# Kernel optimization log

Hardware: AMD Instinct MI355X
Metric: run time of the kernel (lower is better)

Reference implementation:

```python
import jax, jax.numpy as jnp
import numpy as np


def setup_inputs() -> dict:
    B, C, N = 8, 512, 2048
    ks = jax.random.split(jax.random.key(0), 5)
    return {
        "src_embedding": jax.random.normal(ks[0], (B, C, N), jnp.float32),
        "tgt_embedding": jax.random.normal(ks[1], (B, C, N), jnp.float32),
        "src": jax.random.normal(ks[2], (B, 3, N), jnp.float32),
        "tgt": jax.random.normal(ks[3], (B, 3, N), jnp.float32),
        "temperature": jnp.ones((B, 1), jnp.float32),
        "gumbel_u": jax.random.uniform(ks[4], (B * N, N), jnp.float32),
    }


def reference(src_embedding, tgt_embedding, src, tgt, temperature, gumbel_u):
    B, C, N = src_embedding.shape
    # cross-attention scores: [B, N, N]
    scores = jnp.einsum('bcn,bcm->bnm', src_embedding, tgt_embedding) / jnp.sqrt(jnp.float32(C))
    scores = scores.reshape(B * N, N)
    tau = jnp.repeat(temperature.reshape(B, 1, 1), N, axis=1).reshape(-1, 1)  # [B*N, 1]
    # gumbel-softmax (hard=True, straight-through)
    u = jnp.clip(gumbel_u, 1e-6, 1.0 - 1e-6)
    g = -jnp.log(-jnp.log(u))
    y_soft = jax.nn.softmax((scores + g) / tau, axis=-1)
    idx = jnp.argmax(y_soft, axis=-1)
    y_hard = jax.nn.one_hot(idx, N, dtype=y_soft.dtype)
    scores_st = y_hard - jax.lax.stop_gradient(y_soft) + y_soft
    scores_st = scores_st.reshape(B, N, N)
    # soft correspondences: tgt @ scores^T -> [B, 3, N]
    src_corr = jnp.einsum('bcm,bnm->bcn', tgt, scores_st)
    src_mean = src.mean(axis=2, keepdims=True)
    corr_mean = src_corr.mean(axis=2, keepdims=True)
    src_c = src - src_mean
    corr_c = src_corr - corr_mean
    # 3x3 covariance per batch
    H = jnp.einsum('bcn,bdn->bcd', src_c, corr_c)
    uS, s, vh = jnp.linalg.svd(H)
    v = jnp.swapaxes(vh, -1, -2)
    uT = jnp.swapaxes(uS, -1, -2)
    r = v @ uT
    det = jax.lax.stop_gradient(jnp.linalg.det(r))  # torch code uses .item(): constant
    d = jnp.stack([jnp.ones_like(det), jnp.ones_like(det), det], axis=-1)  # [B, 3]
    R = (v * d[:, None, :]) @ uT  # v @ diag([1,1,det]) @ u^T
    t = jnp.einsum('bij,bjk->bik', -R, src_mean) + corr_mean
    return R, t.reshape(B, 3)
```

## Files before the change

### kernel.cpp

```cpp
#include <hip/hip_runtime.h>
#include <hip/hip_fp16.h>
#include <math.h>

#define NB 8
#define NC 512
#define NN 2048

typedef __attribute__((ext_vector_type(8))) _Float16 f16x8;
typedef __attribute__((ext_vector_type(4))) float f32x4;

union U8 { uint32_t u[4]; f16x8 v; };

__device__ __forceinline__ unsigned f2mono(float v) {
    unsigned b = __float_as_uint(v);
    return (b & 0x80000000u) ? ~b : (b | 0x80000000u);
}

__device__ __forceinline__ uint32_t packsplit(float a) {
    __half h = __float2half(a);
    float hf = __half2float(h);
    __half lo = __float2half(a - hf);
    return (uint32_t)__half_as_ushort(h) | ((uint32_t)__half_as_ushort(lo) << 16);
}

__device__ __forceinline__ void g2lds16(const void* g, void* l) {
    __builtin_amdgcn_global_load_lds(
        (const __attribute__((address_space(1))) void*)g,
        (__attribute__((address_space(3))) void*)l, 16, 0, 0);
}

extern "C" __global__ __launch_bounds__(256)
void prepack(const float* __restrict__ srcE, const float* __restrict__ tgtE,
             unsigned short* __restrict__ hiA, unsigned short* __restrict__ loA,
             unsigned short* __restrict__ hiB, unsigned short* __restrict__ loB)
{
    const float* in = blockIdx.y ? tgtE : srcE;
    unsigned short* hi = blockIdx.y ? hiB : hiA;
    unsigned short* lo = blockIdx.y ? loB : loA;
    const int t  = blockIdx.x;
    const int b  = t >> 7;
    const int kt = (t >> 3) & 15;
    const int nt = t & 7;
    const int k0 = kt * 32, n0 = nt * 256;

    const int n_l = threadIdx.x;
    const int n   = n0 + n_l;
    const int s2  = (n >> 1) & 3;
    const float* gin = in + (size_t)b * (NC * NN) + (size_t)k0 * NN + n;

    float v[32];
#pragma unroll
    for (int k = 0; k < 32; ++k) v[k] = gin[(size_t)k * NN];

    uint32_t hw[16], lw[16];
#pragma unroll
    for (int j = 0; j < 16; ++j) {
        __half h0 = __float2half(v[2*j]);
        __half h1 = __float2half(v[2*j+1]);
        float  d0 = v[2*j]   - __half2float(h0);
        float  d1 = v[2*j+1] - __half2float(h1);
        hw[j] = (uint32_t)__half_as_ushort(h0) | ((uint32_t)__half_as_ushort(h1) << 16);
        lw[j] = (uint32_t)__half_as_ushort(__float2half(d0)) |
                ((uint32_t)__half_as_ushort(__float2half(d1)) << 16);
    }
    const size_t rowbase = ((size_t)b * NN + n) * NC;
#pragma unroll
    for (int o = 0; o < 4; ++o) {
        const int P = kt * 4 + (o ^ s2);
        uint4 qh, ql;
        qh.x = hw[4*o+0]; qh.y = hw[4*o+1]; qh.z = hw[4*o+2]; qh.w = hw[4*o+3];
        ql.x = lw[4*o+0]; ql.y = lw[4*o+1]; ql.z = lw[4*o+2]; ql.w = lw[4*o+3];
        *(uint4*)(hi + rowbase + (size_t)P * 8) = qh;
        *(uint4*)(lo + rowbase + (size_t)P * 8) = ql;
    }
}

extern "C" __global__ __launch_bounds__(256, 2)
void scores_argmax_sb(const unsigned short* __restrict__ hiA, const unsigned short* __restrict__ loA,
                      const unsigned short* __restrict__ hiB, const unsigned short* __restrict__ loB,
                      const float* __restrict__ gum,
                      unsigned long long* __restrict__ best)
{
    __shared__ unsigned short lds[4][4096];

    const int id = blockIdx.x;
    const int flat = (id & 7) * 256 + (id >> 3);
    const int mt = flat & 15;
    const int nt = (flat >> 4) & 15;
    const int b  = flat >> 8;
    const int n0 = nt * 128, m0 = mt * 128;

    const int tid = threadIdx.x;
    const int wv = tid >> 6;
    const int l  = tid & 63;
    const int wn = wv >> 1, wm = wv & 1;
    const int row16 = l & 15, h = l >> 4;
    const int s2 = (row16 >> 1) & 3;
    const int fo = (h ^ s2) * 8;

    const unsigned short* gp;
    int pan;
    if (wv == 0)      { gp = hiA; pan = n0; }
    else if (wv == 1) { gp = loA; pan = n0; }
    else if (wv == 2) { gp = hiB; pan = m0; }
    else              { gp = loB; pan = m0; }
    gp += ((size_t)b * NN + pan) * NC;
    const unsigned short* gl = gp + (size_t)(l >> 2) * NC + (l & 3) * 8;

    f32x4 acc[4][4];
#pragma unroll
    for (int i = 0; i < 4; ++i)
#pragma unroll
        for (int j = 0; j < 4; ++j)
            acc[i][j] = (f32x4){0.f, 0.f, 0.f, 0.f};

#pragma unroll 1
    for (int t = 0; t < 16; ++t) {
        __syncthreads();
        {
            const unsigned short* s_ = gl + (size_t)t * 32;
#pragma unroll
            for (int c = 0; c < 8; ++c)
                g2lds16(s_ + (size_t)c * 16 * NC, &lds[wv][c * 512]);
        }
        __syncthreads();

        f16x8 bh[4], bl[4];
#pragma unroll
        for (int ms = 0; ms < 4; ++ms) {
            const int r_ = wm * 64 + ms * 16 + row16;
            bh[ms] = *(const f16x8*)&lds[2][r_ * 32 + fo];
            bl[ms] = *(const f16x8*)&lds[3][r_ * 32 + fo];
        }
#pragma unroll
        for (int ns = 0; ns < 4; ++ns) {
            const int r_ = wn * 64 + ns * 16 + row16;
            const f16x8 ah = *(const f16x8*)&lds[0][r_ * 32 + fo];
            const f16x8 al = *(const f16x8*)&lds[1][r_ * 32 + fo];
#pragma unroll
            for (int ms = 0; ms < 4; ++ms) {
                acc[ns][ms] = __builtin_amdgcn_mfma_f32_16x16x32_f16(ah, bh[ms], acc[ns][ms], 0, 0, 0);
                acc[ns][ms] = __builtin_amdgcn_mfma_f32_16x16x32_f16(al, bh[ms], acc[ns][ms], 0, 0, 0);
                acc[ns][ms] = __builtin_amdgcn_mfma_f32_16x16x32_f16(ah, bl[ms], acc[ns][ms], 0, 0, 0);
            }
        }
    }

    const float SCL = 0.044194173824159216f;
#pragma unroll
    for (int ns = 0; ns < 4; ++ns) {
#pragma unroll
        for (int reg = 0; reg < 4; ++reg) {
            const int n = n0 + wn * 64 + ns * 16 + h * 4 + reg;
            const float* gr = gum + ((size_t)(b * NN + n)) * NN + m0 + wm * 64 + row16;
            unsigned long long bp = 0ULL;
#pragma unroll
            for (int ms = 0; ms < 4; ++ms) {
                float u = gr[ms * 16];
                u = fminf(fmaxf(u, 1e-6f), 1.0f - 1e-6f);
                const float g = -__logf(-__logf(u));
                const float val = fmaf(acc[ns][ms][reg], SCL, g);
                const int m = m0 + wm * 64 + ms * 16 + row16;
                const unsigned long long p =
                    ((unsigned long long)f2mono(val) << 32) | (unsigned)(NN - 1 - m);
                if (p > bp) bp = p;
            }
#pragma unroll
            for (int off = 8; off > 0; off >>= 1) {
                const unsigned long long o = __shfl_xor(bp, off, 16);
                if (o > bp) bp = o;
            }
            if (row16 == 0) atomicMax(&best[(size_t)b * NN + n], bp);
        }
    }
}

extern "C" __global__ __launch_bounds__(256, 2)
void scores_argmax(const float* __restrict__ srcE,
                   const float* __restrict__ tgtE,
                   const float* __restrict__ gum,
                   const float* __restrict__ temp,
                   unsigned long long* __restrict__ best)
{
    __shared__ uint32_t As[128 * 32];
    __shared__ uint32_t Bs[128 * 32];
    const int id = blockIdx.x;
    const int flat = (id & 7) * 256 + (id >> 3);
    const int mt = flat & 15;
    const int nt = (flat >> 4) & 15;
    const int b  = flat >> 8;
    const int n0 = nt * 128, m0 = mt * 128;

    const int tid = threadIdx.x;
    const int wv = tid >> 6;
    const int l  = tid & 63;
    const int wn = wv >> 1, wm = wv & 1;
    const int row16 = l & 15, h = l >> 4;

    const int snb = 4 * (tid & 31);
    const int skb = tid >> 5;
    const uint32_t sswz = (uint32_t)(tid & 7) << 2;

    const float* Ag = srcE + (size_t)b * NC * NN + n0 + snb;
    const float* Bg = tgtE + (size_t)b * NC * NN + m0 + snb;

    float4 pA[4], pB[4];
#pragma unroll
    for (int r = 0; r < 4; ++r) {
        pA[r] = *(const float4*)(Ag + (size_t)(skb + 8 * r) * NN);
        pB[r] = *(const float4*)(Bg + (size_t)(skb + 8 * r) * NN);
    }

    f32x4 acc[4][4];
#pragma unroll
    for (int i = 0; i < 4; ++i)
#pragma unroll
        for (int j = 0; j < 4; ++j)
            acc[i][j] = (f32x4){0.f, 0.f, 0.f, 0.f};

    for (int k0 = 0; k0 < NC; k0 += 32) {
        __syncthreads();
#pragma unroll
        for (int r = 0; r < 4; ++r) {
            const int k = skb + 8 * r;
            const uint32_t kx = (uint32_t)k ^ sswz;
            uint32_t* ap = &As[snb * 32 + kx];
            uint32_t* bq = &Bs[snb * 32 + kx];
            ap[0]  = packsplit(pA[r].x); ap[32] = packsplit(pA[r].y);
            ap[64] = packsplit(pA[r].z); ap[96] = packsplit(pA[r].w);
            bq[0]  = packsplit(pB[r].x); bq[32] = packsplit(pB[r].y);
            bq[64] = packsplit(pB[r].z); bq[96] = packsplit(pB[r].w);
        }
        if (k0 + 32 < NC) {
#pragma unroll
            for (int r = 0; r < 4; ++r) {
                pA[r] = *(const float4*)(Ag + (size_t)(k0 + 32 + skb + 8 * r) * NN);
                pB[r] = *(const float4*)(Bg + (size_t)(k0 + 32 + skb + 8 * r) * NN);
            }
        }
        __syncthreads();

        U8 bfh[4], bfl[4];
#pragma unroll
        for (int ms = 0; ms < 4; ++ms) {
            const int m_loc = wm * 64 + ms * 16 + row16;
            const uint32_t swz = (uint32_t)((ms * 4 + (row16 >> 2)) & 7) << 2;
            const int base = m_loc * 32;
            const uint4 r0 = *(const uint4*)&Bs[base + (((uint32_t)(h * 8 + 0)) ^ swz)];
            const uint4 r1 = *(const uint4*)&Bs[base + (((uint32_t)(h * 8 + 4)) ^ swz)];
            bfh[ms].u[0] = __builtin_amdgcn_perm(r0.y, r0.x, 0x05040100u);
            bfh[ms].u[1] = __builtin_amdgcn_perm(r0.w, r0.z, 0x05040100u);
            bfh[ms].u[2] = __builtin_amdgcn_perm(r1.y, r1.x, 0x05040100u);
            bfh[ms].u[3] = __builtin_amdgcn_perm(r1.w, r1.z, 0x05040100u);
            bfl[ms].u[0] = __builtin_amdgcn_perm(r0.y, r0.x, 0x07060302u);
            bfl[ms].u[1] = __builtin_amdgcn_perm(r0.w, r0.z, 0x07060302u);
            bfl[ms].u[2] = __builtin_amdgcn_perm(r1.y, r1.x, 0x07060302u);
            bfl[ms].u[3] = __builtin_amdgcn_perm(r1.w, r1.z, 0x07060302u);
        }

#pragma unroll
        for (int ns = 0; ns < 4; ++ns) {
            const int n_loc = wn * 64 + ns * 16 + row16;
            const uint32_t swz = (uint32_t)((ns * 4 + (row16 >> 2)) & 7) << 2;
            const int base = n_loc * 32;
            const uint4 r0 = *(const uint4*)&As[base + (((uint32_t)(h * 8 + 0)) ^ swz)];
            const uint4 r1 = *(const uint4*)&As[base + (((uint32_t)(h * 8 + 4)) ^ swz)];
            U8 ah, al;
            ah.u[0] = __builtin_amdgcn_perm(r0.y, r0.x, 0x05040100u);
            ah.u[1] = __builtin_amdgcn_perm(r0.w, r0.z, 0x05040100u);
            ah.u[2] = __builtin_amdgcn_perm(r1.y, r1.x, 0x05040100u);
            ah.u[3] = __builtin_amdgcn_perm(r1.w, r1.z, 0x05040100u);
            al.u[0] = __builtin_amdgcn_perm(r0.y, r0.x, 0x07060302u);
            al.u[1] = __builtin_amdgcn_perm(r0.w, r0.z, 0x07060302u);
            al.u[2] = __builtin_amdgcn_perm(r1.y, r1.x, 0x07060302u);
            al.u[3] = __builtin_amdgcn_perm(r1.w, r1.z, 0x07060302u);
#pragma unroll
            for (int ms = 0; ms < 4; ++ms) {
                acc[ns][ms] = __builtin_amdgcn_mfma_f32_16x16x32_f16(ah.v, bfh[ms].v, acc[ns][ms], 0, 0, 0);
                acc[ns][ms] = __builtin_amdgcn_mfma_f32_16x16x32_f16(al.v, bfh[ms].v, acc[ns][ms], 0, 0, 0);
                acc[ns][ms] = __builtin_amdgcn_mfma_f32_16x16x32_f16(ah.v, bfl[ms].v, acc[ns][ms], 0, 0, 0);
            }
        }
    }

    const float SCL = 0.044194173824159216f;
    const float tau = temp[b];
#pragma unroll
    for (int ns = 0; ns < 4; ++ns) {
#pragma unroll
        for (int reg = 0; reg < 4; ++reg) {
            const int n = n0 + wn * 64 + ns * 16 + h * 4 + reg;
            const float* gr = gum + ((size_t)(b * NN + n)) * NN + m0 + wm * 64 + row16;
            unsigned long long bp = 0ULL;
#pragma unroll
            for (int ms = 0; ms < 4; ++ms) {
                float u = gr[ms * 16];
                u = fminf(fmaxf(u, 1e-6f), 1.0f - 1e-6f);
                const float g = -logf(-logf(u));
                const float val = (acc[ns][ms][reg] * SCL + g) / tau;
                const int m = m0 + wm * 64 + ms * 16 + row16;
                const unsigned long long p =
                    ((unsigned long long)f2mono(val) << 32) | (unsigned)(NN - 1 - m);
                if (p > bp) bp = p;
            }
#pragma unroll
            for (int off = 8; off > 0; off >>= 1) {
                const unsigned long long o = __shfl_xor(bp, off, 16);
                if (o > bp) bp = o;
            }
            if (row16 == 0) atomicMax(&best[(size_t)b * NN + n], bp);
        }
    }
}

__device__ __forceinline__ double det3(const double M[3][3]) {
    return M[0][0] * (M[1][1] * M[2][2] - M[1][2] * M[2][1])
         - M[0][1] * (M[1][0] * M[2][2] - M[1][2] * M[2][0])
         + M[0][2] * (M[1][0] * M[2][1] - M[1][1] * M[2][0]);
}

extern "C" __global__ __launch_bounds__(1024)
void assemble(const float* __restrict__ src, const float* __restrict__ tgt,
              const unsigned long long* __restrict__ best, float* __restrict__ out)
{
    const int b = blockIdx.x;
    const int tid = threadIdx.x;
    float P[9] = {}, Ss[3] = {}, Sc[3] = {};
    for (int n = tid; n < NN; n += 1024) {
        const int m = (NN - 1) - (int)(unsigned)(best[(size_t)b * NN + n] & 0xffffffffu);
        float sv[3], cv[3];
#pragma unroll
        for (int c = 0; c < 3; ++c) {
            sv[c] = src[((size_t)b * 3 + c) * NN + n];
            cv[c] = tgt[((size_t)b * 3 + c) * NN + m];
            Ss[c] += sv[c];
            Sc[c] += cv[c];
        }
#pragma unroll
        for (int c = 0; c < 3; ++c)
#pragma unroll
            for (int d = 0; d < 3; ++d)
                P[c * 3 + d] = fmaf(sv[c], cv[d], P[c * 3 + d]);
    }

    float vals[15];
#pragma unroll
    for (int i = 0; i < 9; ++i) vals[i] = P[i];
#pragma unroll
    for (int i = 0; i < 3; ++i) { vals[9 + i] = Ss[i]; vals[12 + i] = Sc[i]; }

    __shared__ float red[16][15];
    const int lane = tid & 63, wv = tid >> 6;
#pragma unroll
    for (int i = 0; i < 15; ++i) {
        float v = vals[i];
        for (int off = 32; off > 0; off >>= 1) v += __shfl_down(v, off, 64);
        if (lane == 0) red[wv][i] = v;
    }
    __syncthreads();

    if (tid == 0) {
        double tot[15];
        for (int i = 0; i < 15; ++i) {
            double s = 0.0;
            for (int wq = 0; wq < 16; ++wq) s += (double)red[wq][i];
            tot[i] = s;
        }
        double smean[3], cmean[3], H[3][3];
        for (int c = 0; c < 3; ++c) { smean[c] = tot[9 + c] / NN; cmean[c] = tot[12 + c] / NN; }
        for (int c = 0; c < 3; ++c)
            for (int d = 0; d < 3; ++d)
                H[c][d] = tot[c * 3 + d] - tot[9 + c] * tot[12 + d] / NN;

        double W[3][3], V[3][3];
        for (int i = 0; i < 3; ++i)
            for (int j = 0; j < 3; ++j) { W[i][j] = H[i][j]; V[i][j] = (i == j) ? 1.0 : 0.0; }
        for (int sweep = 0; sweep < 60; ++sweep) {
            double offsum = 0.0;
            for (int p = 0; p < 2; ++p)
                for (int q = p + 1; q < 3; ++q) {
                    double al = 0, be = 0, ga = 0;
                    for (int r = 0; r < 3; ++r) {
                        al += W[r][p] * W[r][p];
                        be += W[r][q] * W[r][q];
                        ga += W[r][p] * W[r][q];
                    }
                    offsum += fabs(ga);
                    if (fabs(ga) <= 1e-15 * sqrt(al * be)) continue;
                    double zeta = (be - al) / (2.0 * ga);
                    double t = copysign(1.0, zeta) / (fabs(zeta) + sqrt(1.0 + zeta * zeta));
                    double c = 1.0 / sqrt(1.0 + t * t), s = c * t;
                    for (int r = 0; r < 3; ++r) {
                        double wp = W[r][p], wq = W[r][q];
                        W[r][p] = c * wp - s * wq;
                        W[r][q] = s * wp + c * wq;
                        double vp = V[r][p], vq = V[r][q];
                        V[r][p] = c * vp - s * vq;
                        V[r][q] = s * vp + c * vq;
                    }
                }
            if (offsum < 1e-13) break;
        }
        double S[3];
        for (int i = 0; i < 3; ++i)
            S[i] = sqrt(W[0][i] * W[0][i] + W[1][i] * W[1][i] + W[2][i] * W[2][i]);
        for (int i = 0; i < 2; ++i) {
            int mx = i;
            for (int j = i + 1; j < 3; ++j) if (S[j] > S[mx]) mx = j;
            if (mx != i) {
                double tS = S[i]; S[i] = S[mx]; S[mx] = tS;
                for (int r = 0; r < 3; ++r) {
                    double tw = W[r][i]; W[r][i] = W[r][mx]; W[r][mx] = tw;
                    double tv = V[r][i]; V[r][i] = V[r][mx]; V[r][mx] = tv;
                }
            }
        }
        double U[3][3];
        for (int i = 0; i < 3; ++i) {
            if (S[i] > 1e-12 * S[0] && S[i] > 0.0) {
                for (int r = 0; r < 3; ++r) U[r][i] = W[r][i] / S[i];
            } else {
                double ux = U[1][0] * U[2][1] - U[2][0] * U[1][1];
                double uy = U[2][0] * U[0][1] - U[0][0] * U[2][1];
                double uz = U[0][0] * U[1][1] - U[1][0] * U[0][1];
                double nr = sqrt(ux * ux + uy * uy + uz * uz);
                if (nr < 1e-30) { ux = 1.0; uy = 0.0; uz = 0.0; nr = 1.0; }
                U[0][i] = ux / nr; U[1][i] = uy / nr; U[2][i] = uz / nr;
            }
        }
        double r_[3][3];
        for (int i = 0; i < 3; ++i)
            for (int j = 0; j < 3; ++j)
                r_[i][j] = V[i][0] * U[j][0] + V[i][1] * U[j][1] + V[i][2] * U[j][2];
        double det = det3(r_);
        double R[3][3];
        for (int i = 0; i < 3; ++i)
            for (int j = 0; j < 3; ++j)
                R[i][j] = V[i][0] * U[j][0] + V[i][1] * U[j][1] + det * V[i][2] * U[j][2];
        double t_[3];
        for (int i = 0; i < 3; ++i)
            t_[i] = -(R[i][0] * smean[0] + R[i][1] * smean[1] + R[i][2] * smean[2]) + cmean[i];

        for (int i = 0; i < 3; ++i)
            for (int j = 0; j < 3; ++j)
                out[b * 9 + i * 3 + j] = (float)R[i][j];
        for (int i = 0; i < 3; ++i) out[NB * 9 + b * 3 + i] = (float)t_[i];
    }
}

extern "C" void kernel_launch(void* const* d_in, const int* in_sizes, int n_in,
                              void* d_out, int out_size, void* d_ws, size_t ws_size,
                              hipStream_t stream)
{
    const float* srcE = (const float*)d_in[0];
    const float* tgtE = (const float*)d_in[1];
    const float* src  = (const float*)d_in[2];
    const float* tgt  = (const float*)d_in[3];
    const float* temp = (const float*)d_in[4];
    const float* gum  = (const float*)d_in[5];
    float* out = (float*)d_out;
    unsigned long long* best = (unsigned long long*)d_ws;

    (void)hipMemsetAsync(best, 0, (size_t)NB * NN * sizeof(unsigned long long), stream);

    const size_t PLANE = (size_t)NB * NN * NC;
    const size_t NEED  = 131072 + 4 * PLANE * sizeof(unsigned short);
    if (ws_size >= NEED) {
        unsigned short* hiA = (unsigned short*)((char*)d_ws + 131072);
        unsigned short* loA = hiA + PLANE;
        unsigned short* hiB = loA + PLANE;
        unsigned short* loB = hiB + PLANE;
        prepack<<<dim3(1024, 2), 256, 0, stream>>>(srcE, tgtE, hiA, loA, hiB, loB);
        scores_argmax_sb<<<2048, 256, 0, stream>>>(hiA, loA, hiB, loB, gum, best);
    } else {
        scores_argmax<<<2048, 256, 0, stream>>>(srcE, tgtE, gum, temp, best);
    }
    assemble<<<NB, 1024, 0, stream>>>(src, tgt, best, out);
}
```

Measured before the change: 204.6 us.

## Widen score tile to 256x128 and repack split-fp16 planes k-tile-major

```diff
diff --git a/kernel.cpp b/kernel.cpp
--- a/kernel.cpp
+++ b/kernel.cpp
@@ -63,10 +63,10 @@
         lw[j] = (uint32_t)__half_as_ushort(__float2half(d0)) |
                 ((uint32_t)__half_as_ushort(__float2half(d1)) << 16);
     }
-    const size_t rowbase = ((size_t)b * NN + n) * NC;
+    const size_t rowbase = ((size_t)(b * 16 + kt) * NN + n) * 32;
 #pragma unroll
     for (int o = 0; o < 4; ++o) {
-        const int P = kt * 4 + (o ^ s2);
+        const int P = o ^ s2;
         uint4 qh, ql;
         qh.x = hw[4*o+0]; qh.y = hw[4*o+1]; qh.z = hw[4*o+2]; qh.w = hw[4*o+3];
         ql.x = lw[4*o+0]; ql.y = lw[4*o+1]; ql.z = lw[4*o+2]; ql.w = lw[4*o+3];
@@ -75,41 +75,51 @@
     }
 }
 
+#define PLANE_ELEMS ((uint32_t)NB * NN * NC)
 extern "C" __global__ __launch_bounds__(256, 2)
-void scores_argmax_sb(const unsigned short* __restrict__ hiA, const unsigned short* __restrict__ loA,
-                      const unsigned short* __restrict__ hiB, const unsigned short* __restrict__ loB,
-                      const float* __restrict__ gum,
-                      unsigned long long* __restrict__ best)
+void scores_argmax_wide(const unsigned short* __restrict__ hiA, const unsigned short* __restrict__ loA,
+                        const unsigned short* __restrict__ hiB, const unsigned short* __restrict__ loB,
+                        const float* __restrict__ gum,
+                        unsigned long long* __restrict__ best)
 {
-    __shared__ unsigned short lds[4][4096];
+    __shared__ unsigned short lds[768 * 32];
 
     const int id = blockIdx.x;
-    const int flat = (id & 7) * 256 + (id >> 3);
+    const int flat = (id & 7) * 128 + (id >> 3);
+    const int b  = flat >> 7;
+    const int nt = (flat >> 4) & 7;
     const int mt = flat & 15;
-    const int nt = (flat >> 4) & 15;
-    const int b  = flat >> 8;
-    const int n0 = nt * 128, m0 = mt * 128;
+    const int n0 = nt * 256, m0 = mt * 128;
 
     const int tid = threadIdx.x;
-    const int wv = tid >> 6;
-    const int l  = tid & 63;
-    const int wn = wv >> 1, wm = wv & 1;
+    const int w = tid >> 6;
+    const int l = tid & 63;
+    const int wn = w >> 1, wm = w & 1;
     const int row16 = l & 15, h = l >> 4;
     const int s2 = (row16 >> 1) & 3;
     const int fo = (h ^ s2) * 8;
 
-    const unsigned short* gp;
-    int pan;
-    if (wv == 0)      { gp = hiA; pan = n0; }
-    else if (wv == 1) { gp = loA; pan = n0; }
-    else if (wv == 2) { gp = hiB; pan = m0; }
-    else              { gp = loB; pan = m0; }
-    gp += ((size_t)b * NN + pan) * NC;
-    const unsigned short* gl = gp + (size_t)(l >> 2) * NC + (l & 3) * 8;
-
-    f32x4 acc[4][4];
-#pragma unroll
-    for (int i = 0; i < 4; ++i)
+#define MKOFF(j) uint32_t off##j; { \
+    const int gr_ = w * 192 + (j) * 16; \
+    int plane_, prow_, pan_; \
+    if (gr_ < 256)      { plane_ = 0; prow_ = gr_;       pan_ = n0; } \
+    else if (gr_ < 512) { plane_ = 1; prow_ = gr_ - 256; pan_ = n0; } \
+    else if (gr_ < 640) { plane_ = 2; prow_ = gr_ - 512; pan_ = m0; } \
+    else                { plane_ = 3; prow_ = gr_ - 640; pan_ = m0; } \
+    off##j = plane_ * PLANE_ELEMS + \
+             (uint32_t)(((b * 16) * NN + pan_ + prow_ + (l >> 2)) * 32 + (l & 3) * 8); \
+}
+    MKOFF(0) MKOFF(1) MKOFF(2) MKOFF(3) MKOFF(4) MKOFF(5)
+    MKOFF(6) MKOFF(7) MKOFF(8) MKOFF(9) MKOFF(10) MKOFF(11)
+#undef MKOFF
+
+    unsigned short* ldsw = &lds[w * 192 * 32];
+
+#define STGJ(T, j) g2lds16(hiA + off##j + (uint32_t)(T) * (NN * 32), ldsw + (j) * 512)
+
+    f32x4 acc[8][4];
+#pragma unroll
+    for (int i = 0; i < 8; ++i)
 #pragma unroll
         for (int j = 0; j < 4; ++j)
             acc[i][j] = (f32x4){0.f, 0.f, 0.f, 0.f};
@@ -117,26 +127,23 @@
 #pragma unroll 1
     for (int t = 0; t < 16; ++t) {
         __syncthreads();
-        {
-            const unsigned short* s_ = gl + (size_t)t * 32;
-#pragma unroll
-            for (int c = 0; c < 8; ++c)
-                g2lds16(s_ + (size_t)c * 16 * NC, &lds[wv][c * 512]);
-        }
+        STGJ(t, 0);  STGJ(t, 1);  STGJ(t, 2);  STGJ(t, 3);
+        STGJ(t, 4);  STGJ(t, 5);  STGJ(t, 6);  STGJ(t, 7);
+        STGJ(t, 8);  STGJ(t, 9);  STGJ(t, 10); STGJ(t, 11);
         __syncthreads();
 
         f16x8 bh[4], bl[4];
 #pragma unroll
         for (int ms = 0; ms < 4; ++ms) {
-            const int r_ = wm * 64 + ms * 16 + row16;
-            bh[ms] = *(const f16x8*)&lds[2][r_ * 32 + fo];
-            bl[ms] = *(const f16x8*)&lds[3][r_ * 32 + fo];
-        }
-#pragma unroll
-        for (int ns = 0; ns < 4; ++ns) {
-            const int r_ = wn * 64 + ns * 16 + row16;
-            const f16x8 ah = *(const f16x8*)&lds[0][r_ * 32 + fo];
-            const f16x8 al = *(const f16x8*)&lds[1][r_ * 32 + fo];
+            const int rB = wm * 64 + ms * 16 + row16;
+            bh[ms] = *(const f16x8*)&lds[(512 + rB) * 32 + fo];
+            bl[ms] = *(const f16x8*)&lds[(640 + rB) * 32 + fo];
+        }
+#pragma unroll
+        for (int ns = 0; ns < 8; ++ns) {
+            const int rA = wn * 128 + ns * 16 + row16;
+            const f16x8 ah = *(const f16x8*)&lds[rA * 32 + fo];
+            const f16x8 al = *(const f16x8*)&lds[(256 + rA) * 32 + fo];
 #pragma unroll
             for (int ms = 0; ms < 4; ++ms) {
                 acc[ns][ms] = __builtin_amdgcn_mfma_f32_16x16x32_f16(ah, bh[ms], acc[ns][ms], 0, 0, 0);
@@ -145,13 +152,14 @@
             }
         }
     }
+#undef STGJ
 
     const float SCL = 0.044194173824159216f;
 #pragma unroll
-    for (int ns = 0; ns < 4; ++ns) {
+    for (int ns = 0; ns < 8; ++ns) {
 #pragma unroll
         for (int reg = 0; reg < 4; ++reg) {
-            const int n = n0 + wn * 64 + ns * 16 + h * 4 + reg;
+            const int n = n0 + wn * 128 + ns * 16 + h * 4 + reg;
             const float* gr = gum + ((size_t)(b * NN + n)) * NN + m0 + wm * 64 + row16;
             unsigned long long bp = 0ULL;
 #pragma unroll
@@ -471,7 +479,7 @@
         unsigned short* hiB = loA + PLANE;
         unsigned short* loB = hiB + PLANE;
         prepack<<<dim3(1024, 2), 256, 0, stream>>>(srcE, tgtE, hiA, loA, hiB, loB);
-        scores_argmax_sb<<<2048, 256, 0, stream>>>(hiA, loA, hiB, loB, gum, best);
+        scores_argmax_wide<<<1024, 256, 0, stream>>>(hiA, loA, hiB, loB, gum, best);
     } else {
         scores_argmax<<<2048, 256, 0, stream>>>(srcE, tgtE, gum, temp, best);
     }
```

Result: slower. 208.9 us (+2.1%).
